# Optimization experiments

Hardware: AMD Instinct MI355X
Metric: run time of the kernel (lower is better)

The kernel has to match this reference:

```python
import jax, jax.numpy as jnp
import numpy as np

N = 50000   # nodes per graph
E = 500000  # edges per graph
F_IN = 128  # num_features
H = 128     # hidden_channels
C = 64      # num_classes
G = 64      # graphs per batch
NEG_SLOPE = 0.2


def setup_inputs() -> dict:
    key = jax.random.key(0)
    ks = jax.random.split(key, 16)
    s = 1.0 / np.sqrt(H)
    return {
        "x1": jax.random.normal(ks[0], (N, F_IN), jnp.float32),
        "x2": jax.random.normal(ks[1], (N, F_IN), jnp.float32),
        # stacked params for the 2 GATConv layers (F_IN == H so shapes match)
        "convW": jax.random.normal(ks[2], (2, H, H), jnp.float32) * s,
        "att_src": jax.random.normal(ks[3], (2, H), jnp.float32) * s,
        "att_dst": jax.random.normal(ks[4], (2, H), jnp.float32) * s,
        "conv_b": jnp.zeros((2, H), jnp.float32),
        "mlp_w1": jax.random.normal(ks[5], (H, H), jnp.float32) * s,
        "mlp_b1": jnp.zeros((H,), jnp.float32),
        "mlp_w2": jax.random.normal(ks[6], (H, C), jnp.float32) * s,
        "mlp_b2": jnp.zeros((C,), jnp.float32),
        "edge_index1": jax.random.randint(ks[7], (2, E), 0, N, jnp.int64),
        "batch1": jnp.sort(jax.random.randint(ks[8], (N,), 0, G, jnp.int64)),
        "edge_index2": jax.random.randint(ks[9], (2, E), 0, N, jnp.int64),
        "batch2": jnp.sort(jax.random.randint(ks[10], (N,), 0, G, jnp.int64)),
    }


def gat_conv(x, src, dst, W, a_s, a_d, b):
    # PyG GATConv, heads=1, add_self_loops already applied in src/dst
    n = x.shape[0]
    h = x @ W                                   # [N, H]
    alpha_s = h @ a_s                           # [N]
    alpha_d = h @ a_d                           # [N]
    e = alpha_s[src] + alpha_d[dst]             # [Etot]
    e = jnp.where(e > 0, e, NEG_SLOPE * e)      # leaky_relu
    # segment softmax over incoming edges of each dst node
    m = jax.ops.segment_max(e, dst, num_segments=n)
    ex = jnp.exp(e - m[dst])
    denom = jax.ops.segment_sum(ex, dst, num_segments=n)
    alpha = ex / denom[dst]                     # [Etot]
    out = jax.ops.segment_sum(h[src] * alpha[:, None], dst, num_segments=n)
    return out + b


def reference(x1, x2, convW, att_src, att_dst, conv_b,
              mlp_w1, mlp_b1, mlp_w2, mlp_b2,
              edge_index1, batch1, edge_index2, batch2):
    def branch(x, ei):
        n = x.shape[0]
        loops = jnp.arange(n, dtype=ei.dtype)
        src = jnp.concatenate([ei[0], loops])
        dst = jnp.concatenate([ei[1], loops])
        # num_layers=3 -> 2 convs; i != num_layers-1 always true -> ELU after each
        for l in range(2):
            x = gat_conv(x, src, dst, convW[l], att_src[l], att_dst[l], conv_b[l])
            x = jax.nn.elu(x)
            # dropout p=0.5 is identity in eval mode
        return jax.nn.relu(x @ mlp_w1 + mlp_b1) @ mlp_w2 + mlp_b2

    h1 = branch(x1, edge_index1)
    h2 = branch(x2, edge_index2)
    p1 = jax.ops.segment_sum(h1, batch1, num_segments=G)  # [G, C]
    p2 = jax.ops.segment_sum(h2, batch2, num_segments=G)  # [G, C]
    return p1.T @ p2                                      # [C, C]
```

## Files before the change

kernel.cpp:

```cpp
#include <hip/hip_runtime.h>
#include <cstdint>
#include <cstddef>

#define NNODES 50000
#define NEDGES 500000
#define NTOT (NEDGES + NNODES)
#define HDIM 128
#define CDIM 64
#define GDIM 64
#define NB 250
#define NPB 200
#define CHUNK 2048
#define NCHB ((NEDGES + CHUNK - 1) / CHUNK)

typedef __bf16 bf16x8 __attribute__((ext_vector_type(8)));
typedef float f32x4 __attribute__((ext_vector_type(4)));


__global__ __launch_bounds__(256) void k_setup(const float* __restrict__ convW,
                                               const float* __restrict__ w1,
                                               const float* __restrict__ w2,
                                               const float* __restrict__ a_s,
                                               const float* __restrict__ a_d,
                                               __bf16* __restrict__ WtC,
                                               __bf16* __restrict__ Wt1,
                                               __bf16* __restrict__ Wt2,
                                               float* __restrict__ Wa,
                                               float* __restrict__ p) {
    int b = blockIdx.x, tid = threadIdx.x;
    if (b < 128) {
        int i = b * 256 + tid;
        int mat = i >> 14, rem = i & 16383;
        int k = rem >> 7, n = rem & 127;
        WtC[mat * 16384 + n * 128 + k] = (__bf16)convW[i];
    } else if (b < 192) {
        int i = (b - 128) * 256 + tid;
        int k = i >> 7, n = i & 127;
        Wt1[n * 128 + k] = (__bf16)w1[i];
    } else if (b < 224) {
        int i = (b - 192) * 256 + tid;
        int k = i >> 6, n = i & 63;
        Wt2[n * 128 + k] = (__bf16)w2[i];
    } else if (b == 224) {
        for (int o = tid; o < 512; o += 256) {
            int l = o >> 8, r = o & 255;
            int type = r >> 7, k = r & 127;
            const float* a = (type ? a_d : a_s) + l * 128;
            const float* Wrow = convW + l * 16384 + k * 128;
            float s = 0.f;
            for (int j = 0; j < 128; j++) s += Wrow[j] * a[j];
            Wa[o] = s;
        }
    } else {
        for (int i = tid; i < 2 * GDIM * CDIM; i += 256) p[i] = 0.f;
    }
}


__global__ __launch_bounds__(256) void k_bhist(const int* __restrict__ ei0,
                                               const int* __restrict__ ei1,
                                               int* __restrict__ bcntB, int e) {
    __shared__ int h[NB];
    const int* dst = (blockIdx.y ? ei1 : ei0) + NEDGES;
    int* bcnt = bcntB + blockIdx.y * NB;
    for (int t = threadIdx.x; t < NB; t += 256) h[t] = 0;
    __syncthreads();
    int base = blockIdx.x * CHUNK;
    int lim = min(base + CHUNK, e);
    for (int i = base + threadIdx.x; i < lim; i += 256) atomicAdd(&h[dst[i] / NPB], 1);
    __syncthreads();
    for (int t = threadIdx.x; t < NB; t += 256)
        if (h[t]) atomicAdd(&bcnt[t], h[t]);
}

__global__ __launch_bounds__(256) void k_bscan(const int* __restrict__ bcntB,
                                               int* __restrict__ boffB,
                                               int* __restrict__ bcurB) {
    __shared__ int s[256];
    int t = threadIdx.x;
    const int* bcnt = bcntB + blockIdx.y * NB;
    int* boff = boffB + blockIdx.y * (NB + 1);
    int* bcur = bcurB + blockIdx.y * NB;
    int v = (t < NB) ? bcnt[t] : 0;
    s[t] = v;
    __syncthreads();
    for (int off = 1; off < 256; off <<= 1) {
        int x = (t >= off) ? s[t - off] : 0;
        __syncthreads();
        s[t] += x;
        __syncthreads();
    }
    if (t < NB) {
        boff[t + 1] = s[t];
        bcur[t] = s[t] - v;
        if (t == 0) boff[0] = 0;
    }
}

__global__ __launch_bounds__(256) void k_part(const int* __restrict__ ei0,
                                              const int* __restrict__ ei1,
                                              int* __restrict__ bcurB,
                                              int2* __restrict__ partB, int e) {
    __shared__ int cnt[NB], boffL[NB], gbase[NB], cur2[NB];
    __shared__ int tmp[256];
    __shared__ int2 staged[CHUNK];
    const int* eis = blockIdx.y ? ei1 : ei0;
    int* bcur = bcurB + blockIdx.y * NB;
    int2* part = partB + blockIdx.y * (size_t)NEDGES;
    int t = threadIdx.x;
    for (int i = t; i < NB; i += 256) { cnt[i] = 0; cur2[i] = 0; }
    __syncthreads();
    int base = blockIdx.x * CHUNK;
    int lim = min(base + CHUNK, e);
    int nloc = lim - base;

    int s_[8], d_[8], b_[8];
    bool v_[8];
#pragma unroll
    for (int k = 0; k < 8; k++) {
        int i = base + k * 256 + t;
        v_[k] = i < lim;
        s_[k] = 0; d_[k] = 0; b_[k] = 0;
        if (v_[k]) {
            s_[k] = eis[i];
            d_[k] = eis[NEDGES + i];
            b_[k] = d_[k] / NPB;
            atomicAdd(&cnt[b_[k]], 1);
        }
    }
    __syncthreads();
    tmp[t] = (t < NB) ? cnt[t] : 0;
    __syncthreads();
    for (int off = 1; off < 256; off <<= 1) {
        int x = (t >= off) ? tmp[t - off] : 0;
        __syncthreads();
        tmp[t] += x;
        __syncthreads();
    }
    if (t < NB) boffL[t] = tmp[t] - cnt[t];
    __syncthreads();
    if (t < NB) {
        int c = cnt[t];
        gbase[t] = c ? atomicAdd(&bcur[t], c) : 0;
    }
    __syncthreads();
#pragma unroll
    for (int k = 0; k < 8; k++) {
        if (v_[k]) {
            int pos = atomicAdd(&cur2[b_[k]], 1);
            staged[boffL[b_[k]] + pos] = make_int2(s_[k], d_[k]);
        }
    }
    __syncthreads();
    for (int i = t; i < nloc; i += 256) {
        int2 r = staged[i];
        int b = r.y / NPB;
        part[gbase[b] + (i - boffL[b])] = r;
    }
}

__global__ __launch_bounds__(256) void k_bdeg(const int2* __restrict__ partB,
                                              const int* __restrict__ boffB,
                                              int* __restrict__ degB, size_t sN) {
    __shared__ int h[NPB];
    int b = blockIdx.x;
    const int* boff = boffB + blockIdx.y * (NB + 1);
    const int2* part = partB + blockIdx.y * (size_t)NEDGES;
    int* deg = degB + blockIdx.y * sN;
    int t = threadIdx.x;
    if (t < NPB) h[t] = 0;
    __syncthreads();
    int beg = boff[b], end = boff[b + 1];
    int n0 = b * NPB;
    for (int i = beg + t; i < end; i += 256) atomicAdd(&h[part[i].y - n0], 1);
    __syncthreads();
    if (t < NPB) deg[n0 + t] = h[t];
}

__device__ inline int block_scan_incl(int v, int* lds) {
    int lane = threadIdx.x & 63, wid = threadIdx.x >> 6;
#pragma unroll
    for (int off = 1; off < 64; off <<= 1) {
        int nv = __shfl_up(v, off);
        if (lane >= off) v += nv;
    }
    if (lane == 63) lds[wid] = v;
    __syncthreads();
    if (wid == 0) {
        int s = (lane < 16) ? lds[lane] : 0;
#pragma unroll
        for (int off = 1; off < 16; off <<= 1) {
            int nv = __shfl_up(s, off);
            if (lane >= off) s += nv;
        }
        if (lane < 16) lds[lane] = s;
    }
    __syncthreads();
    return (wid > 0) ? v + lds[wid - 1] : v;
}

__global__ __launch_bounds__(1024) void k_scan1(const int* __restrict__ degB, int* __restrict__ inclB,
                                                int* __restrict__ bsumsB, size_t sN, int n) {
    __shared__ int lds[16];
    const int* deg = degB + blockIdx.y * sN;
    int* incl = inclB + blockIdx.y * sN;
    int* bsums = bsumsB + blockIdx.y * 64;
    int i = blockIdx.x * 1024 + threadIdx.x;
    int v = (i < n) ? deg[i] : 0;
    int s = block_scan_incl(v, lds);
    if (i < n) incl[i] = s;
    if (threadIdx.x == 1023) bsums[blockIdx.x] = s;
}

__global__ void k_scan2(int* __restrict__ bsumsB, int nb) {
    int* bsums = bsumsB + blockIdx.y * 64;
    int lane = threadIdx.x;
    int v = (lane < nb) ? bsums[lane] : 0;
#pragma unroll
    for (int off = 1; off < 64; off <<= 1) {
        int nv = __shfl_up(v, off);
        if (lane >= off) v += nv;
    }
    if (lane < nb) bsums[lane] = v;
}

__global__ __launch_bounds__(1024) void k_scan3(const int* __restrict__ inclB,
                                                const int* __restrict__ bsumsB, int* __restrict__ rpB,
                                                size_t sN, size_t sNp1, int n) {
    int i = blockIdx.x * 1024 + threadIdx.x;
    if (i >= n) return;
    const int* incl = inclB + blockIdx.y * sN;
    const int* bsums = bsumsB + blockIdx.y * 64;
    int* row_ptr = rpB + blockIdx.y * sNp1;
    int off = (blockIdx.x > 0) ? bsums[blockIdx.x - 1] : 0;
    row_ptr[i + 1] = incl[i] + off + i + 1;
    if (i == 0) row_ptr[0] = 0;
}

__global__ __launch_bounds__(256) void k_place(const int2* __restrict__ partB,
                                               const int* __restrict__ boffB,
                                               const int* __restrict__ rpB, size_t sNp1,
                                               int* __restrict__ colB, size_t sE) {
    __shared__ int cur[NPB];
    int b = blockIdx.x;
    const int* boff = boffB + blockIdx.y * (NB + 1);
    const int2* part = partB + blockIdx.y * (size_t)NEDGES;
    const int* row_ptr = rpB + blockIdx.y * sNp1;
    int* col = colB + blockIdx.y * sE;
    int t = threadIdx.x;
    int n0 = b * NPB;
    if (t < NPB) {
        int rp = row_ptr[n0 + t];
        cur[t] = rp + 1;
        col[rp] = n0 + t;
    }
    __syncthreads();
    int beg = boff[b], end = boff[b + 1];
    for (int i = beg + t; i < end; i += 256) {
        int2 r = part[i];
        int p = atomicAdd(&cur[r.y - n0], 1);
        col[p] = r.x;
    }
}


template <int BN, int MODE, bool AF32, bool ALPHA>
__global__ __launch_bounds__(256) void k_gemm_mfma(const float* __restrict__ x0,
                                                   const float* __restrict__ x1,
                                                   const __bf16* __restrict__ Ab, size_t As_,
                                                   const __bf16* __restrict__ Wt,
                                                   const float* __restrict__ bias,
                                                   const float* __restrict__ Was,
                                                   const float* __restrict__ Wad,
                                                   float* __restrict__ asB, float* __restrict__ adB,
                                                   size_t aS,
                                                   __bf16* __restrict__ OutB, size_t Os_, int M) {
    constexpr int WAVES_N = (BN == 128) ? 2 : 1;
    constexpr int WAVES_M = 4 / WAVES_N;
    constexpr int WM = 64 / WAVES_M;
    constexpr int MF = WM / 16;
    constexpr int NF = 4;
    __shared__ __align__(16) unsigned short As[64][136];
    __shared__ __align__(16) unsigned short Bs[BN][136];
    const int tid = threadIdx.x;
    const int lane = tid & 63, w = tid >> 6;
    const int row0 = blockIdx.x * 64;
    __bf16* Out = OutB + blockIdx.y * Os_;

#pragma unroll
    for (int t = 0; t < 4; t++) {
        int ch = t * 256 + tid;
        int r = ch >> 4, cx = ch & 15;
        int grow = row0 + r;
        bf16x8 v = {};
        if (grow < M) {
            if (AF32) {
                const float* Ap = (blockIdx.y ? x1 : x0) + (size_t)grow * 128 + cx * 8;
                float4 f0 = *reinterpret_cast<const float4*>(Ap);
                float4 f1 = *reinterpret_cast<const float4*>(Ap + 4);
                v[0] = (__bf16)f0.x; v[1] = (__bf16)f0.y; v[2] = (__bf16)f0.z; v[3] = (__bf16)f0.w;
                v[4] = (__bf16)f1.x; v[5] = (__bf16)f1.y; v[6] = (__bf16)f1.z; v[7] = (__bf16)f1.w;
            } else {
                v = *reinterpret_cast<const bf16x8*>(Ab + blockIdx.y * As_ + (size_t)grow * 128 + cx * 8);
            }
        }
        *reinterpret_cast<bf16x8*>(&As[r][cx * 8]) = v;
    }
#pragma unroll
    for (int t = 0; t < BN / 16; t++) {
        int ch = t * 256 + tid;
        int r = ch >> 4, cx = ch & 15;
        bf16x8 v = *reinterpret_cast<const bf16x8*>(Wt + (size_t)r * 128 + cx * 8);
        *reinterpret_cast<bf16x8*>(&Bs[r][cx * 8]) = v;
    }
    __syncthreads();

    if (ALPHA) {
        int row = tid >> 2, seg = tid & 3;
        float ss = 0.f, sd = 0.f;
#pragma unroll
        for (int k = 0; k < 32; k++) {
            int kk = seg * 32 + k;
            float a = __int_as_float(((unsigned)As[row][kk]) << 16);
            ss += a * Was[kk];
            sd += a * Wad[kk];
        }
        ss += __shfl_xor(ss, 1); ss += __shfl_xor(ss, 2);
        sd += __shfl_xor(sd, 1); sd += __shfl_xor(sd, 2);
        if (seg == 0) {
            int grow = row0 + row;
            if (grow < M) {
                (asB + blockIdx.y * aS)[grow] = ss;
                (adB + blockIdx.y * aS)[grow] = sd;
            }
        }
    }

    const int wr0 = (w / WAVES_N) * WM;
    const int wc0 = (w % WAVES_N) * 64;
    f32x4 acc[MF][NF] = {};

#pragma unroll
    for (int ks = 0; ks < 4; ks++) {
        const int koff = ks * 32 + (lane >> 4) * 8;
        bf16x8 af[MF], bfr[NF];
#pragma unroll
        for (int mf = 0; mf < MF; mf++)
            af[mf] = *reinterpret_cast<const bf16x8*>(&As[wr0 + mf * 16 + (lane & 15)][koff]);
#pragma unroll
        for (int nf = 0; nf < NF; nf++)
            bfr[nf] = *reinterpret_cast<const bf16x8*>(&Bs[wc0 + nf * 16 + (lane & 15)][koff]);
#pragma unroll
        for (int mf = 0; mf < MF; mf++)
#pragma unroll
            for (int nf = 0; nf < NF; nf++)
                acc[mf][nf] = __builtin_amdgcn_mfma_f32_16x16x32_bf16(af[mf], bfr[nf], acc[mf][nf], 0, 0, 0);
    }

#pragma unroll
    for (int mf = 0; mf < MF; mf++) {
#pragma unroll
        for (int r = 0; r < 4; r++) {
            int row = row0 + wr0 + mf * 16 + (lane >> 4) * 4 + r;
            if (row >= M) continue;
#pragma unroll
            for (int nf = 0; nf < NF; nf++) {
                int colc = wc0 + nf * 16 + (lane & 15);
                float v = acc[mf][nf][r];
                if (MODE == 1) v = fmaxf(v + bias[colc], 0.f);
                if (MODE == 2) v = v + bias[colc];
                Out[(size_t)row * BN + colc] = (__bf16)v;
            }
        }
    }
}


__global__ __launch_bounds__(256) void k_gat_agg(const __bf16* __restrict__ hB, size_t hS,
                                                 const float* __restrict__ asB,
                                                 const float* __restrict__ adB, size_t aS,
                                                 const int* __restrict__ rpB, size_t sNp1,
                                                 const int* __restrict__ colB, size_t sE,
                                                 const float* __restrict__ bias,
                                                 __bf16* __restrict__ outB, size_t oS, int n) {
    int node = blockIdx.x * 4 + (threadIdx.x >> 6);
    int lane = threadIdx.x & 63;
    if (node >= n) return;
    const float* alpha_s = asB + blockIdx.y * aS;
    const int* row_ptr = rpB + blockIdx.y * sNp1;
    const int* col = colB + blockIdx.y * sE;
    const bf16x8* h8 = reinterpret_cast<const bf16x8*>(hB + blockIdx.y * hS);
    float ad = (adB + blockIdx.y * aS)[node];
    int beg = row_ptr[node], end = row_ptr[node + 1];
    int deg = end - beg;
    int sub = lane >> 4, fo = lane & 15;

    float acc[8] = {0.f, 0.f, 0.f, 0.f, 0.f, 0.f, 0.f, 0.f};

    if (deg <= 64) {
        bool v = lane < deg;
        int c = 0;
        float e = -1e30f;
        if (v) {
            c = col[beg + lane];
            e = alpha_s[c] + ad;
            e = (e > 0.f) ? e : 0.2f * e;
        }
        float m = e;
#pragma unroll
        for (int off = 32; off; off >>= 1) m = fmaxf(m, __shfl_xor(m, off));
        float ex = v ? __expf(e - m) : 0.f;
        float den = ex;
#pragma unroll
        for (int off = 32; off; off >>= 1) den += __shfl_xor(den, off);
        float wn = ex / den;

        int nIter = (deg + 3) >> 2;
        int k = sub;
        for (int t = 0; t < nIter; t += 2) {
            int k1 = k & 63, k2 = (k + 4) & 63;
            int c1 = __shfl(c, k1); float w1 = __shfl(wn, k1);
            int c2 = __shfl(c, k2); float w2 = __shfl(wn, k2);
            bool v1 = k < deg, v2 = (k + 4) < deg;
            w1 = v1 ? w1 : 0.f; c1 = v1 ? c1 : 0;
            w2 = v2 ? w2 : 0.f; c2 = v2 ? c2 : 0;
            bf16x8 h1 = h8[(size_t)c1 * 16 + fo];
            bf16x8 h2 = h8[(size_t)c2 * 16 + fo];
#pragma unroll
            for (int q = 0; q < 8; q++) acc[q] += w1 * (float)h1[q] + w2 * (float)h2[q];
            k += 8;
        }
    } else {
        float m = -1e30f;
        for (int i = beg + lane; i < end; i += 64) {
            float e = alpha_s[col[i]] + ad;
            e = (e > 0.f) ? e : 0.2f * e;
            m = fmaxf(m, e);
        }
#pragma unroll
        for (int off = 32; off; off >>= 1) m = fmaxf(m, __shfl_xor(m, off));
        float den = 0.f;
        for (int i = beg + lane; i < end; i += 64) {
            float e = alpha_s[col[i]] + ad;
            e = (e > 0.f) ? e : 0.2f * e;
            den += __expf(e - m);
        }
#pragma unroll
        for (int off = 32; off; off >>= 1) den += __shfl_xor(den, off);
        float rinv = 1.f / den;
        for (int i = beg + sub; i < end; i += 4) {
            int cc = col[i];
            float e = alpha_s[cc] + ad;
            e = (e > 0.f) ? e : 0.2f * e;
            float wv = __expf(e - m) * rinv;
            bf16x8 hv = h8[(size_t)cc * 16 + fo];
#pragma unroll
            for (int q = 0; q < 8; q++) acc[q] += wv * (float)hv[q];
        }
    }

#pragma unroll
    for (int q = 0; q < 8; q++) {
        acc[q] += __shfl_xor(acc[q], 16);
        acc[q] += __shfl_xor(acc[q], 32);
    }
    if (sub == 0) {
        float4 b0 = reinterpret_cast<const float4*>(bias)[fo * 2];
        float4 b1 = reinterpret_cast<const float4*>(bias)[fo * 2 + 1];
        float vb[8] = {acc[0] + b0.x, acc[1] + b0.y, acc[2] + b0.z, acc[3] + b0.w,
                       acc[4] + b1.x, acc[5] + b1.y, acc[6] + b1.z, acc[7] + b1.w};
        bf16x8 o;
#pragma unroll
        for (int q = 0; q < 8; q++) {
            float x = vb[q];
            x = (x > 0.f) ? x : __expf(x) - 1.f;
            o[q] = (__bf16)x;
        }
        reinterpret_cast<bf16x8*>(outB + blockIdx.y * oS)[(size_t)node * 16 + fo] = o;
    }
}


__global__ __launch_bounds__(64) void k_pool(const __bf16* __restrict__ uB, size_t uS,
                                             const int* __restrict__ bat0, const int* __restrict__ bat1,
                                             float* __restrict__ pB, size_t pS, int n) {
    int lane = threadIdx.x;
    const __bf16* u = uB + blockIdx.y * uS;
    const int* batch = blockIdx.y ? bat1 : bat0;
    float* p = pB + blockIdx.y * pS;
    int base = blockIdx.x * 64;
    int endn = min(base + 64, n);
    float acc = 0.f;
    int cur = -1;
    for (int nn = base; nn < endn; ++nn) {
        int g = batch[nn];
        if (g != cur) {
            if (cur >= 0) atomicAdd(&p[cur * CDIM + lane], acc);
            acc = 0.f;
            cur = g;
        }
        acc += (float)u[(size_t)nn * CDIM + lane];
    }
    if (cur >= 0) atomicAdd(&p[cur * CDIM + lane], acc);
}


__global__ __launch_bounds__(64) void k_final(const float* __restrict__ p, float* __restrict__ out) {
    int i = blockIdx.x;
    int j = threadIdx.x;
    const float* p1 = p;
    const float* p2 = p + GDIM * CDIM;
    float s = 0.f;
    for (int g = 0; g < GDIM; ++g) s += p1[g * CDIM + i] * p2[g * CDIM + j];
    out[i * CDIM + j] = s;
}


static inline size_t align_up(size_t x, size_t a) { return (x + a - 1) & ~(a - 1); }

struct Ws {
    __bf16 *Hb, *Yb, *U;
    __bf16 *WtC, *Wt1, *Wt2;
    float *alpha_s, *alpha_d, *Wa, *p;
    int *deg, *incl, *row_ptr, *bsums, *col;
    int *bcnt, *boff, *bcur;
    int2* part;
    size_t sNH, sNC, sN, sNp1, sE;
    size_t need;
};

static Ws carve(void* ws, bool combined) {
    char* p = (char*)ws;
    size_t off = 0;
    Ws w;
    int nb = combined ? 2 : 1;
    auto take = [&](size_t bytes) {
        char* r = p + off;
        off = align_up(off + bytes, 256);
        return r;
    };
    w.Hb = (__bf16*)take((size_t)nb * NNODES * HDIM * 2);
    w.Yb = (__bf16*)take((size_t)nb * NNODES * HDIM * 2);
    w.U = (__bf16*)take((size_t)nb * NNODES * CDIM * 2);
    w.alpha_s = (float*)take((size_t)nb * NNODES * 4);
    w.alpha_d = (float*)take((size_t)nb * NNODES * 4);
    w.col = (int*)take((size_t)nb * NTOT * 4);
    w.part = (int2*)take((size_t)nb * NEDGES * 8);
    w.deg = (int*)take((size_t)nb * NNODES * 4);
    w.incl = (int*)take((size_t)nb * NNODES * 4);
    w.row_ptr = (int*)take((size_t)nb * (NNODES + 1) * 4);
    w.bsums = (int*)take((size_t)2 * 64 * 4);
    w.bcnt = (int*)take((size_t)2 * NB * 4);
    w.boff = (int*)take((size_t)2 * (NB + 1) * 4);
    w.bcur = (int*)take((size_t)2 * NB * 4);
    w.WtC = (__bf16*)take((size_t)2 * HDIM * HDIM * 2);
    w.Wt1 = (__bf16*)take((size_t)HDIM * HDIM * 2);
    w.Wt2 = (__bf16*)take((size_t)HDIM * CDIM * 2);
    w.Wa = (float*)take((size_t)512 * 4);
    w.p = (float*)take((size_t)2 * GDIM * CDIM * 4);
    w.need = off;
    size_t s = combined ? 1 : 0;
    w.sNH = s * (size_t)NNODES * HDIM;
    w.sNC = s * (size_t)NNODES * CDIM;
    w.sN = s * (size_t)NNODES;
    w.sNp1 = s * (size_t)(NNODES + 1);
    w.sE = s * (size_t)NTOT;
    return w;
}

static void pipeline(const Ws& w, const float* xA, const float* xB,
                     const int* eiA, const int* eiB,
                     const int* batA, const int* batB,
                     const float* conv_b, const float* b1, const float* b2,
                     float* pbase, size_t pstride, int yc, hipStream_t stream) {
    const int N = NNODES, E = NEDGES;
    int nb = (N + 1023) / 1024;
    dim3 gC(NCHB, yc), gB(NB, yc), g1(1, yc), gS(nb, yc);
    dim3 gW((N + 3) / 4, yc);
    dim3 gG((N + 63) / 64, yc);
    dim3 gP((N + 63) / 64, yc);

    hipMemsetAsync(w.bcnt, 0, (size_t)yc * NB * 4, stream);
    k_bhist<<<gC, 256, 0, stream>>>(eiA, eiB, w.bcnt, E);
    k_bscan<<<g1, 256, 0, stream>>>(w.bcnt, w.boff, w.bcur);
    k_part<<<gC, 256, 0, stream>>>(eiA, eiB, w.bcur, w.part, E);
    k_bdeg<<<gB, 256, 0, stream>>>(w.part, w.boff, w.deg, w.sN);
    k_scan1<<<gS, 1024, 0, stream>>>(w.deg, w.incl, w.bsums, w.sN, N);
    k_scan2<<<g1, 64, 0, stream>>>(w.bsums, nb);
    k_scan3<<<gS, 1024, 0, stream>>>(w.incl, w.bsums, w.row_ptr, w.sN, w.sNp1, N);
    k_place<<<gB, 256, 0, stream>>>(w.part, w.boff, w.row_ptr, w.sNp1, w.col, w.sE);

    k_gemm_mfma<HDIM, 0, true, true><<<gG, 256, 0, stream>>>(
        xA, xB, nullptr, 0, w.WtC, nullptr, w.Wa, w.Wa + 128,
        w.alpha_s, w.alpha_d, w.sN, w.Hb, w.sNH, N);
    k_gat_agg<<<gW, 256, 0, stream>>>(w.Hb, w.sNH, w.alpha_s, w.alpha_d, w.sN,
                                      w.row_ptr, w.sNp1, w.col, w.sE, conv_b, w.Yb, w.sNH, N);
    k_gemm_mfma<HDIM, 0, false, true><<<gG, 256, 0, stream>>>(
        nullptr, nullptr, w.Yb, w.sNH, w.WtC + HDIM * HDIM, nullptr, w.Wa + 256, w.Wa + 384,
        w.alpha_s, w.alpha_d, w.sN, w.Hb, w.sNH, N);
    k_gat_agg<<<gW, 256, 0, stream>>>(w.Hb, w.sNH, w.alpha_s, w.alpha_d, w.sN,
                                      w.row_ptr, w.sNp1, w.col, w.sE, conv_b + HDIM, w.Yb, w.sNH, N);
    k_gemm_mfma<HDIM, 1, false, false><<<gG, 256, 0, stream>>>(
        nullptr, nullptr, w.Yb, w.sNH, w.Wt1, b1, nullptr, nullptr,
        nullptr, nullptr, 0, w.Hb, w.sNH, N);
    k_gemm_mfma<CDIM, 2, false, false><<<gG, 256, 0, stream>>>(
        nullptr, nullptr, w.Hb, w.sNH, w.Wt2, b2, nullptr, nullptr,
        nullptr, nullptr, 0, w.U, w.sNC, N);

    k_pool<<<gP, 64, 0, stream>>>(w.U, w.sNC, batA, batB, pbase, pstride, N);
}

extern "C" void kernel_launch(void* const* d_in, const int* in_sizes, int n_in, void* d_out,
                              int out_size, void* d_ws, size_t ws_size, hipStream_t stream) {
    const float* x1      = (const float*)d_in[0];
    const float* x2      = (const float*)d_in[1];
    const float* convW   = (const float*)d_in[2];
    const float* att_src = (const float*)d_in[3];
    const float* att_dst = (const float*)d_in[4];
    const float* conv_b  = (const float*)d_in[5];
    const float* mlp_w1  = (const float*)d_in[6];
    const float* mlp_b1  = (const float*)d_in[7];
    const float* mlp_w2  = (const float*)d_in[8];
    const float* mlp_b2  = (const float*)d_in[9];
    const int* ei1       = (const int*)d_in[10];
    const int* batch1    = (const int*)d_in[11];
    const int* ei2       = (const int*)d_in[12];
    const int* batch2    = (const int*)d_in[13];
    float* out = (float*)d_out;

    Ws wc = carve(d_ws, true);
    bool combined = ws_size >= wc.need;
    Ws w = combined ? wc : carve(d_ws, false);

    k_setup<<<226, 256, 0, stream>>>(convW, mlp_w1, mlp_w2, att_src, att_dst,
                                     w.WtC, w.Wt1, w.Wt2, w.Wa, w.p);

    if (combined) {
        pipeline(w, x1, x2, ei1, ei2, batch1, batch2, conv_b,
                 mlp_b1, mlp_b2, w.p, (size_t)GDIM * CDIM, 2, stream);
    } else {
        pipeline(w, x1, x1, ei1, ei1, batch1, batch1, conv_b,
                 mlp_b1, mlp_b2, w.p, 0, 1, stream);
        pipeline(w, x2, x2, ei2, ei2, batch2, batch2, conv_b,
                 mlp_b1, mlp_b2, w.p + GDIM * CDIM, 0, 1, stream);
    }

    k_final<<<CDIM, 64, 0, stream>>>(w.p, out);
}
```

Measured before the change: 374.9 us.

## Fuse MLP GEMMs and graph pooling into one kernel; spread aggregation epilogue

```diff
diff --git a/kernel.cpp b/kernel.cpp
--- a/kernel.cpp
+++ b/kernel.cpp
@@ -14,6 +14,7 @@
 #define NCHB ((NEDGES + CHUNK - 1) / CHUNK)
 
 typedef __bf16 bf16x8 __attribute__((ext_vector_type(8)));
+typedef __bf16 bf16x2 __attribute__((ext_vector_type(2)));
 typedef float f32x4 __attribute__((ext_vector_type(4)));
 
 
@@ -264,22 +265,17 @@
 }
 
 
-template <int BN, int MODE, bool AF32, bool ALPHA>
-__global__ __launch_bounds__(256) void k_gemm_mfma(const float* __restrict__ x0,
+template <bool AF32>
+__global__ __launch_bounds__(256) void k_gemm_conv(const float* __restrict__ x0,
                                                    const float* __restrict__ x1,
                                                    const __bf16* __restrict__ Ab, size_t As_,
                                                    const __bf16* __restrict__ Wt,
-                                                   const float* __restrict__ bias,
                                                    const float* __restrict__ Was,
                                                    const float* __restrict__ Wad,
                                                    float* __restrict__ asB, float* __restrict__ adB,
                                                    size_t aS,
                                                    __bf16* __restrict__ OutB, size_t Os_, int M) {
-    constexpr int WAVES_N = (BN == 128) ? 2 : 1;
-    constexpr int WAVES_M = 4 / WAVES_N;
-    constexpr int WM = 64 / WAVES_M;
-    constexpr int MF = WM / 16;
-    constexpr int NF = 4;
+    constexpr int BN = 128;
     __shared__ __align__(16) unsigned short As[64][136];
     __shared__ __align__(16) unsigned short Bs[BN][136];
     const int tid = threadIdx.x;
@@ -307,7 +303,7 @@
         *reinterpret_cast<bf16x8*>(&As[r][cx * 8]) = v;
     }
 #pragma unroll
-    for (int t = 0; t < BN / 16; t++) {
+    for (int t = 0; t < 8; t++) {
         int ch = t * 256 + tid;
         int r = ch >> 4, cx = ch & 15;
         bf16x8 v = *reinterpret_cast<const bf16x8*>(Wt + (size_t)r * 128 + cx * 8);
@@ -315,7 +311,7 @@
     }
     __syncthreads();
 
-    if (ALPHA) {
+    {
         int row = tid >> 2, seg = tid & 3;
         float ss = 0.f, sd = 0.f;
 #pragma unroll
@@ -336,40 +332,37 @@
         }
     }
 
-    const int wr0 = (w / WAVES_N) * WM;
-    const int wc0 = (w % WAVES_N) * 64;
-    f32x4 acc[MF][NF] = {};
+    const int wr0 = (w >> 1) * 32;
+    const int wc0 = (w & 1) * 64;
+    f32x4 acc[2][4] = {};
 
 #pragma unroll
     for (int ks = 0; ks < 4; ks++) {
         const int koff = ks * 32 + (lane >> 4) * 8;
-        bf16x8 af[MF], bfr[NF];
-#pragma unroll
-        for (int mf = 0; mf < MF; mf++)
+        bf16x8 af[2], bfr[4];
+#pragma unroll
+        for (int mf = 0; mf < 2; mf++)
             af[mf] = *reinterpret_cast<const bf16x8*>(&As[wr0 + mf * 16 + (lane & 15)][koff]);
 #pragma unroll
-        for (int nf = 0; nf < NF; nf++)
+        for (int nf = 0; nf < 4; nf++)
             bfr[nf] = *reinterpret_cast<const bf16x8*>(&Bs[wc0 + nf * 16 + (lane & 15)][koff]);
 #pragma unroll
-        for (int mf = 0; mf < MF; mf++)
-#pragma unroll
-            for (int nf = 0; nf < NF; nf++)
+        for (int mf = 0; mf < 2; mf++)
+#pragma unroll
+            for (int nf = 0; nf < 4; nf++)
                 acc[mf][nf] = __builtin_amdgcn_mfma_f32_16x16x32_bf16(af[mf], bfr[nf], acc[mf][nf], 0, 0, 0);
     }
 
 #pragma unroll
-    for (int mf = 0; mf < MF; mf++) {
+    for (int mf = 0; mf < 2; mf++) {
 #pragma unroll
         for (int r = 0; r < 4; r++) {
             int row = row0 + wr0 + mf * 16 + (lane >> 4) * 4 + r;
             if (row >= M) continue;
 #pragma unroll
-            for (int nf = 0; nf < NF; nf++) {
+            for (int nf = 0; nf < 4; nf++) {
                 int colc = wc0 + nf * 16 + (lane & 15);
-                float v = acc[mf][nf][r];
-                if (MODE == 1) v = fmaxf(v + bias[colc], 0.f);
-                if (MODE == 2) v = v + bias[colc];
-                Out[(size_t)row * BN + colc] = (__bf16)v;
+                Out[(size_t)row * BN + colc] = (__bf16)acc[mf][nf][r];
             }
         }
     }
@@ -389,11 +382,12 @@
     const float* alpha_s = asB + blockIdx.y * aS;
     const int* row_ptr = rpB + blockIdx.y * sNp1;
     const int* col = colB + blockIdx.y * sE;
-    const bf16x8* h8 = reinterpret_cast<const bf16x8*>(hB + blockIdx.y * hS);
+    const char* hbase = (const char*)(hB + blockIdx.y * hS);
     float ad = (adB + blockIdx.y * aS)[node];
     int beg = row_ptr[node], end = row_ptr[node + 1];
     int deg = end - beg;
     int sub = lane >> 4, fo = lane & 15;
+    int foff = fo * 16;
 
     float acc[8] = {0.f, 0.f, 0.f, 0.f, 0.f, 0.f, 0.f, 0.f};
 
@@ -424,8 +418,8 @@
             bool v1 = k < deg, v2 = (k + 4) < deg;
             w1 = v1 ? w1 : 0.f; c1 = v1 ? c1 : 0;
             w2 = v2 ? w2 : 0.f; c2 = v2 ? c2 : 0;
-            bf16x8 h1 = h8[(size_t)c1 * 16 + fo];
-            bf16x8 h2 = h8[(size_t)c2 * 16 + fo];
+            bf16x8 h1 = *reinterpret_cast<const bf16x8*>(hbase + (c1 << 8) + foff);
+            bf16x8 h2 = *reinterpret_cast<const bf16x8*>(hbase + (c2 << 8) + foff);
 #pragma unroll
             for (int q = 0; q < 8; q++) acc[q] += w1 * (float)h1[q] + w2 * (float)h2[q];
             k += 8;
@@ -453,7 +447,7 @@
             float e = alpha_s[cc] + ad;
             e = (e > 0.f) ? e : 0.2f * e;
             float wv = __expf(e - m) * rinv;
-            bf16x8 hv = h8[(size_t)cc * 16 + fo];
+            bf16x8 hv = *reinterpret_cast<const bf16x8*>(hbase + (cc << 8) + foff);
 #pragma unroll
             for (int q = 0; q < 8; q++) acc[q] += wv * (float)hv[q];
         }
@@ -464,44 +458,140 @@
         acc[q] += __shfl_xor(acc[q], 16);
         acc[q] += __shfl_xor(acc[q], 32);
     }
-    if (sub == 0) {
-        float4 b0 = reinterpret_cast<const float4*>(bias)[fo * 2];
-        float4 b1 = reinterpret_cast<const float4*>(bias)[fo * 2 + 1];
-        float vb[8] = {acc[0] + b0.x, acc[1] + b0.y, acc[2] + b0.z, acc[3] + b0.w,
-                       acc[4] + b1.x, acc[5] + b1.y, acc[6] + b1.z, acc[7] + b1.w};
-        bf16x8 o;
-#pragma unroll
-        for (int q = 0; q < 8; q++) {
-            float x = vb[q];
-            x = (x > 0.f) ? x : __expf(x) - 1.f;
-            o[q] = (__bf16)x;
-        }
-        reinterpret_cast<bf16x8*>(outB + blockIdx.y * oS)[(size_t)node * 16 + fo] = o;
-    }
-}
-
-
-__global__ __launch_bounds__(64) void k_pool(const __bf16* __restrict__ uB, size_t uS,
-                                             const int* __restrict__ bat0, const int* __restrict__ bat1,
-                                             float* __restrict__ pB, size_t pS, int n) {
-    int lane = threadIdx.x;
-    const __bf16* u = uB + blockIdx.y * uS;
+    float2 bv = *reinterpret_cast<const float2*>(bias + fo * 8 + 2 * sub);
+    float x0 = (sub & 2) ? ((sub & 1) ? acc[6] : acc[4]) : ((sub & 1) ? acc[2] : acc[0]);
+    float x1 = (sub & 2) ? ((sub & 1) ? acc[7] : acc[5]) : ((sub & 1) ? acc[3] : acc[1]);
+    x0 += bv.x; x1 += bv.y;
+    x0 = (x0 > 0.f) ? x0 : __expf(x0) - 1.f;
+    x1 = (x1 > 0.f) ? x1 : __expf(x1) - 1.f;
+    bf16x2 ov;
+    ov.x = (__bf16)x0; ov.y = (__bf16)x1;
+    char* ob = (char*)(outB + blockIdx.y * oS) + ((unsigned)node << 8) + foff + sub * 4;
+    *reinterpret_cast<unsigned int*>(ob) = __builtin_bit_cast(unsigned int, ov);
+}
+
+
+__global__ __launch_bounds__(256) void k_mlp_pool(const __bf16* __restrict__ AbB, size_t As_,
+                                                  const __bf16* __restrict__ Wt1,
+                                                  const __bf16* __restrict__ Wt2,
+                                                  const float* __restrict__ b1,
+                                                  const float* __restrict__ b2,
+                                                  const int* __restrict__ bat0,
+                                                  const int* __restrict__ bat1,
+                                                  float* __restrict__ pB, size_t pS, int M) {
+    __shared__ __align__(16) unsigned short As[64][136];
+    __shared__ __align__(16) unsigned short Bs[128][136];
+    const int tid = threadIdx.x;
+    const int lane = tid & 63, w = tid >> 6;
+    const int row0 = blockIdx.x * 64;
+    const __bf16* Ab = AbB + blockIdx.y * As_;
     const int* batch = blockIdx.y ? bat1 : bat0;
     float* p = pB + blockIdx.y * pS;
-    int base = blockIdx.x * 64;
-    int endn = min(base + 64, n);
-    float acc = 0.f;
-    int cur = -1;
-    for (int nn = base; nn < endn; ++nn) {
-        int g = batch[nn];
-        if (g != cur) {
-            if (cur >= 0) atomicAdd(&p[cur * CDIM + lane], acc);
-            acc = 0.f;
-            cur = g;
-        }
-        acc += (float)u[(size_t)nn * CDIM + lane];
-    }
-    if (cur >= 0) atomicAdd(&p[cur * CDIM + lane], acc);
+
+#pragma unroll
+    for (int t = 0; t < 4; t++) {
+        int ch = t * 256 + tid;
+        int r = ch >> 4, cx = ch & 15;
+        int grow = row0 + r;
+        bf16x8 v = {};
+        if (grow < M) v = *reinterpret_cast<const bf16x8*>(Ab + (size_t)grow * 128 + cx * 8);
+        *reinterpret_cast<bf16x8*>(&As[r][cx * 8]) = v;
+    }
+#pragma unroll
+    for (int t = 0; t < 8; t++) {
+        int ch = t * 256 + tid;
+        int r = ch >> 4, cx = ch & 15;
+        bf16x8 v = *reinterpret_cast<const bf16x8*>(Wt1 + (size_t)r * 128 + cx * 8);
+        *reinterpret_cast<bf16x8*>(&Bs[r][cx * 8]) = v;
+    }
+    __syncthreads();
+
+    {
+        const int wr0 = (w >> 1) * 32;
+        const int wc0 = (w & 1) * 64;
+        f32x4 acc[2][4] = {};
+#pragma unroll
+        for (int ks = 0; ks < 4; ks++) {
+            const int koff = ks * 32 + (lane >> 4) * 8;
+            bf16x8 af[2], bfr[4];
+#pragma unroll
+            for (int mf = 0; mf < 2; mf++)
+                af[mf] = *reinterpret_cast<const bf16x8*>(&As[wr0 + mf * 16 + (lane & 15)][koff]);
+#pragma unroll
+            for (int nf = 0; nf < 4; nf++)
+                bfr[nf] = *reinterpret_cast<const bf16x8*>(&Bs[wc0 + nf * 16 + (lane & 15)][koff]);
+#pragma unroll
+            for (int mf = 0; mf < 2; mf++)
+#pragma unroll
+                for (int nf = 0; nf < 4; nf++)
+                    acc[mf][nf] = __builtin_amdgcn_mfma_f32_16x16x32_bf16(af[mf], bfr[nf], acc[mf][nf], 0, 0, 0);
+        }
+        __syncthreads();
+#pragma unroll
+        for (int mf = 0; mf < 2; mf++)
+#pragma unroll
+            for (int r = 0; r < 4; r++) {
+                int row = wr0 + mf * 16 + (lane >> 4) * 4 + r;
+#pragma unroll
+                for (int nf = 0; nf < 4; nf++) {
+                    int colc = wc0 + nf * 16 + (lane & 15);
+                    float v = fmaxf(acc[mf][nf][r] + b1[colc], 0.f);
+                    As[row][colc] = __builtin_bit_cast(unsigned short, (__bf16)v);
+                }
+            }
+#pragma unroll
+        for (int t = 0; t < 4; t++) {
+            int ch = t * 256 + tid;
+            int r = ch >> 4, cx = ch & 15;
+            bf16x8 v = *reinterpret_cast<const bf16x8*>(Wt2 + (size_t)r * 128 + cx * 8);
+            *reinterpret_cast<bf16x8*>(&Bs[r][cx * 8]) = v;
+        }
+        __syncthreads();
+    }
+
+    const int wr2 = w * 16;
+    f32x4 acc2[4] = {};
+#pragma unroll
+    for (int ks = 0; ks < 4; ks++) {
+        const int koff = ks * 32 + (lane >> 4) * 8;
+        bf16x8 a2 = *reinterpret_cast<const bf16x8*>(&As[wr2 + (lane & 15)][koff]);
+#pragma unroll
+        for (int nf = 0; nf < 4; nf++) {
+            bf16x8 bf2 = *reinterpret_cast<const bf16x8*>(&Bs[nf * 16 + (lane & 15)][koff]);
+            acc2[nf] = __builtin_amdgcn_mfma_f32_16x16x32_bf16(a2, bf2, acc2[nf], 0, 0, 0);
+        }
+    }
+
+    int q = lane >> 4, c = lane & 15;
+    bool full = (row0 + 63) < M;
+    int g0 = batch[min(row0, M - 1)];
+    int g1 = batch[min(row0 + 63, M - 1)];
+    if (full && g0 == g1) {
+        float s0 = acc2[0][0] + acc2[0][1] + acc2[0][2] + acc2[0][3];
+        float s1 = acc2[1][0] + acc2[1][1] + acc2[1][2] + acc2[1][3];
+        float s2 = acc2[2][0] + acc2[2][1] + acc2[2][2] + acc2[2][3];
+        float s3 = acc2[3][0] + acc2[3][1] + acc2[3][2] + acc2[3][3];
+        s0 += __shfl_xor(s0, 16); s0 += __shfl_xor(s0, 32);
+        s1 += __shfl_xor(s1, 16); s1 += __shfl_xor(s1, 32);
+        s2 += __shfl_xor(s2, 16); s2 += __shfl_xor(s2, 32);
+        s3 += __shfl_xor(s3, 16); s3 += __shfl_xor(s3, 32);
+        float v = (q & 2) ? ((q & 1) ? s3 : s2) : ((q & 1) ? s1 : s0);
+        v += 16.f * b2[q * 16 + c];
+        atomicAdd(&p[g0 * CDIM + q * 16 + c], v);
+    } else {
+        float b2v[4];
+#pragma unroll
+        for (int nf = 0; nf < 4; nf++) b2v[nf] = b2[nf * 16 + c];
+#pragma unroll
+        for (int r = 0; r < 4; r++) {
+            int row = row0 + wr2 + q * 4 + r;
+            if (row >= M) continue;
+            int g = batch[row];
+#pragma unroll
+            for (int nf = 0; nf < 4; nf++)
+                atomicAdd(&p[g * CDIM + nf * 16 + c], acc2[nf][r] + b2v[nf]);
+        }
+    }
 }
 
 
@@ -519,13 +609,13 @@
 static inline size_t align_up(size_t x, size_t a) { return (x + a - 1) & ~(a - 1); }
 
 struct Ws {
-    __bf16 *Hb, *Yb, *U;
+    __bf16 *Hb, *Yb;
     __bf16 *WtC, *Wt1, *Wt2;
     float *alpha_s, *alpha_d, *Wa, *p;
     int *deg, *incl, *row_ptr, *bsums, *col;
     int *bcnt, *boff, *bcur;
     int2* part;
-    size_t sNH, sNC, sN, sNp1, sE;
+    size_t sNH, sN, sNp1, sE;
     size_t need;
 };
 
@@ -541,7 +631,6 @@
     };
     w.Hb = (__bf16*)take((size_t)nb * NNODES * HDIM * 2);
     w.Yb = (__bf16*)take((size_t)nb * NNODES * HDIM * 2);
-    w.U = (__bf16*)take((size_t)nb * NNODES * CDIM * 2);
     w.alpha_s = (float*)take((size_t)nb * NNODES * 4);
     w.alpha_d = (float*)take((size_t)nb * NNODES * 4);
     w.col = (int*)take((size_t)nb * NTOT * 4);
@@ -561,7 +650,6 @@
     w.need = off;
     size_t s = combined ? 1 : 0;
     w.sNH = s * (size_t)NNODES * HDIM;
-    w.sNC = s * (size_t)NNODES * CDIM;
     w.sN = s * (size_t)NNODES;
     w.sNp1 = s * (size_t)(NNODES + 1);
     w.sE = s * (size_t)NTOT;
@@ -578,7 +666,6 @@
     dim3 gC(NCHB, yc), gB(NB, yc), g1(1, yc), gS(nb, yc);
     dim3 gW((N + 3) / 4, yc);
     dim3 gG((N + 63) / 64, yc);
-    dim3 gP((N + 63) / 64, yc);
 
     hipMemsetAsync(w.bcnt, 0, (size_t)yc * NB * 4, stream);
     k_bhist<<<gC, 256, 0, stream>>>(eiA, eiB, w.bcnt, E);
@@ -590,24 +677,18 @@
     k_scan3<<<gS, 1024, 0, stream>>>(w.incl, w.bsums, w.row_ptr, w.sN, w.sNp1, N);
     k_place<<<gB, 256, 0, stream>>>(w.part, w.boff, w.row_ptr, w.sNp1, w.col, w.sE);
 
-    k_gemm_mfma<HDIM, 0, true, true><<<gG, 256, 0, stream>>>(
-        xA, xB, nullptr, 0, w.WtC, nullptr, w.Wa, w.Wa + 128,
+    k_gemm_conv<true><<<gG, 256, 0, stream>>>(
+        xA, xB, nullptr, 0, w.WtC, w.Wa, w.Wa + 128,
         w.alpha_s, w.alpha_d, w.sN, w.Hb, w.sNH, N);
     k_gat_agg<<<gW, 256, 0, stream>>>(w.Hb, w.sNH, w.alpha_s, w.alpha_d, w.sN,
                                       w.row_ptr, w.sNp1, w.col, w.sE, conv_b, w.Yb, w.sNH, N);
-    k_gemm_mfma<HDIM, 0, false, true><<<gG, 256, 0, stream>>>(
-        nullptr, nullptr, w.Yb, w.sNH, w.WtC + HDIM * HDIM, nullptr, w.Wa + 256, w.Wa + 384,
+    k_gemm_conv<false><<<gG, 256, 0, stream>>>(
+        nullptr, nullptr, w.Yb, w.sNH, w.WtC + HDIM * HDIM, w.Wa + 256, w.Wa + 384,
         w.alpha_s, w.alpha_d, w.sN, w.Hb, w.sNH, N);
     k_gat_agg<<<gW, 256, 0, stream>>>(w.Hb, w.sNH, w.alpha_s, w.alpha_d, w.sN,
                                       w.row_ptr, w.sNp1, w.col, w.sE, conv_b + HDIM, w.Yb, w.sNH, N);
-    k_gemm_mfma<HDIM, 1, false, false><<<gG, 256, 0, stream>>>(
-        nullptr, nullptr, w.Yb, w.sNH, w.Wt1, b1, nullptr, nullptr,
-        nullptr, nullptr, 0, w.Hb, w.sNH, N);
-    k_gemm_mfma<CDIM, 2, false, false><<<gG, 256, 0, stream>>>(
-        nullptr, nullptr, w.Hb, w.sNH, w.Wt2, b2, nullptr, nullptr,
-        nullptr, nullptr, 0, w.U, w.sNC, N);
-
-    k_pool<<<gP, 64, 0, stream>>>(w.U, w.sNC, batA, batB, pbase, pstride, N);
+    k_mlp_pool<<<gG, 256, 0, stream>>>(w.Yb, w.sNH, w.Wt1, w.Wt2, b1, b2,
+                                       batA, batB, pbase, pstride, N);
 }
 
 extern "C" void kernel_launch(void* const* d_in, const int* in_sizes, int n_in, void* d_out,
```

Result: faster. 347.0 us (-7.5%).
